# Kernel optimization log

Hardware: AMD Instinct MI355X
Metric: run time of the kernel (lower is better)

## Reference

```python
import jax, jax.numpy as jnp
import numpy as np

B, T, C, H = 4, 2048, 1024, 16
HD = C // H  # head dim = 64


def setup_inputs() -> dict:
    key = jax.random.key(0)
    ks = jax.random.split(key, 5)
    s = 1.0 / np.sqrt(C)
    return {
        "x": jax.random.normal(ks[0], (B, T, C), jnp.float32),
        "Wk": jax.random.normal(ks[1], (C, C), jnp.float32) * s,
        "bk": jnp.zeros((C,), jnp.float32),
        "Wq": jax.random.normal(ks[2], (C, C), jnp.float32) * s,
        "bq": jnp.zeros((C,), jnp.float32),
        "Wv": jax.random.normal(ks[3], (C, C), jnp.float32) * s,
        "bv": jnp.zeros((C,), jnp.float32),
        "Wp": jax.random.normal(ks[4], (C, C), jnp.float32) * s,
        "bp": jnp.zeros((C,), jnp.float32),
    }


def reference(x, Wk, bk, Wq, bq, Wv, bv, Wp, bp):
    # Linear(in, out): y = x @ W.T + b  (W stored as [out, in], torch convention)
    k = (x @ Wk.T + bk).reshape(B, T, H, HD).transpose(0, 2, 1, 3)  # [B,H,T,HD]
    q = (x @ Wq.T + bq).reshape(B, T, H, HD).transpose(0, 2, 1, 3)
    v = (x @ Wv.T + bv).reshape(B, T, H, HD).transpose(0, 2, 1, 3)
    scale = 1.0 / np.sqrt(HD)
    att = jnp.einsum("bhqd,bhkd->bhqk", q, k) * scale  # [B,H,T,T]
    causal = jnp.tril(jnp.ones((T, T), bool))
    att = jnp.where(causal[None, None, :, :], att, -jnp.inf)
    att = jax.nn.softmax(att, axis=-1)
    y = jnp.einsum("bhqk,bhkd->bhqd", att, v)  # [B,H,T,HD]
    y = y.transpose(0, 2, 1, 3).reshape(B, T, C)
    return y @ Wp.T + bp
```

## Files before the change

kernel.cpp:

```cpp
#include <hip/hip_runtime.h>
#include <hip/hip_bf16.h>
#include <cmath>

#define Tt 2048
#define Cc 1024
#define Hh 16
#define HDd 64

typedef __attribute__((ext_vector_type(8))) short short8;
typedef __attribute__((ext_vector_type(4))) float f32x4;

#define ASYNC16(gp, lp)                                       \
    __builtin_amdgcn_global_load_lds(                         \
        (const __attribute__((address_space(1))) void*)(gp),  \
        (__attribute__((address_space(3))) void*)(lp), 16, 0, 0)

__device__ __forceinline__ unsigned short f32_bf16(float f) {
    unsigned u = __float_as_uint(f);
    u += 0x7FFF + ((u >> 16) & 1);
    return (unsigned short)(u >> 16);
}
__device__ __forceinline__ unsigned short f32_bf16_rn(float f) {
    return (unsigned short)((__float_as_uint(f) + 0x8000u) >> 16);
}
__device__ __forceinline__ float fast_exp2(float x) {
#if __has_builtin(__builtin_amdgcn_exp2f)
    return __builtin_amdgcn_exp2f(x);
#else
    return exp2f(x);
#endif
}

__global__ __launch_bounds__(256) void cvt_all(
    const float* __restrict__ x, const float* __restrict__ a,
    const float* __restrict__ b, const float* __restrict__ c,
    const float* __restrict__ d, unsigned short* __restrict__ ox,
    unsigned short* __restrict__ oa, unsigned short* __restrict__ ob,
    unsigned short* __restrict__ oc, unsigned short* __restrict__ od) {
    const int id = blockIdx.x * 256 + threadIdx.x;
    const float* src; unsigned short* dst; int sub;
    if (id < 2097152) {
        src = x; dst = ox; sub = id;
    } else {
        const int wi = id - 2097152;
        const int which = wi >> 18;
        sub = wi & 262143;
        if (which == 0)      { src = a; dst = oa; }
        else if (which == 1) { src = b; dst = ob; }
        else if (which == 2) { src = c; dst = oc; }
        else                 { src = d; dst = od; }
    }
    float4 v = ((const float4*)src)[sub];
    ushort4 o;
    o.x = f32_bf16(v.x); o.y = f32_bf16(v.y);
    o.z = f32_bf16(v.z); o.w = f32_bf16(v.w);
    ((ushort4*)dst)[sub] = o;
}

__global__ __launch_bounds__(512, 2) void gemm_qkv8(
    const unsigned short* __restrict__ A,
    const unsigned short* __restrict__ Wcat,
    const float* __restrict__ bq, const float* __restrict__ bk,
    const float* __restrict__ bv,
    unsigned short* __restrict__ qout, unsigned short* __restrict__ kout,
    unsigned short* __restrict__ vout) {
    extern __shared__ unsigned short lds[];

    const int tid  = threadIdx.x;
    const int wid  = tid >> 6;
    const int lane = tid & 63;
    const int quad = lane >> 4;
    const int lr   = lane & 15;
    const int wr   = wid >> 2;
    const int wc   = wid & 3;

    const int bm0 = blockIdx.y * 256;
    const int bn0 = blockIdx.x * 256;

    const int srow  = wid * 8 + (lane >> 3);
    const int scol  = ((lane & 7) ^ (lane >> 3)) * 8;
    const int sldso = wid * 512;

    const int a_r   = wr * 64 + lr;
    const int b_r   = wc * 32 + lr;
    const int slot0 = (quad ^ (lr & 7)) * 8;
    const int slot1 = ((quad ^ 4) ^ (lr & 7)) * 8;

    f32x4 acc[8][4];
    const f32x4 zero = {0.f, 0.f, 0.f, 0.f};
#pragma unroll
    for (int i = 0; i < 8; ++i)
#pragma unroll
        for (int j = 0; j < 4; ++j) acc[i][j] = zero;

    short8 areg[4][2];
    short8 breg[2][2][2];

#define STG(S, BUF, REG, GB, GROW)                                          \
    do {                                                                    \
        if ((S) < 16) {                                                     \
            unsigned short* lb = lds + ((BUF) * 4 + (REG)) * 8192 + sldso;  \
            const unsigned short* gp =                                      \
                (GB) + (size_t)((GROW) + srow) * Cc + (S) * 64 + scol;      \
            ASYNC16(gp, lb);                                                \
            ASYNC16(gp + (size_t)64 * Cc, lb + 4096);                       \
        }                                                                   \
    } while (0)

#define LDA(mh)                                                             \
    do {                                                                    \
        const unsigned short* ab = bufb + (mh) * 8192;                      \
        _Pragma("unroll") for (int mf = 0; mf < 4; ++mf) {                  \
            areg[mf][0] = *(const short8*)(ab + (a_r + mf * 16) * 64 + slot0); \
            areg[mf][1] = *(const short8*)(ab + (a_r + mf * 16) * 64 + slot1); \
        }                                                                   \
    } while (0)

#define LDB(nh)                                                             \
    do {                                                                    \
        const unsigned short* bb = bufb + (2 + (nh)) * 8192;                \
        _Pragma("unroll") for (int nf = 0; nf < 2; ++nf) {                  \
            breg[nh][nf][0] = *(const short8*)(bb + (b_r + nf * 16) * 64 + slot0); \
            breg[nh][nf][1] = *(const short8*)(bb + (b_r + nf * 16) * 64 + slot1); \
        }                                                                   \
    } while (0)

#define MFMA_PHASE(mh, nh)                                                  \
    _Pragma("unroll") for (int mf = 0; mf < 4; ++mf)                        \
    _Pragma("unroll") for (int nf = 0; nf < 2; ++nf) {                      \
        acc[(mh)*4+mf][(nh)*2+nf] = __builtin_amdgcn_mfma_f32_16x16x32_bf16( \
            areg[mf][0], breg[nh][nf][0], acc[(mh)*4+mf][(nh)*2+nf], 0,0,0); \
        acc[(mh)*4+mf][(nh)*2+nf] = __builtin_amdgcn_mfma_f32_16x16x32_bf16( \
            areg[mf][1], breg[nh][nf][1], acc[(mh)*4+mf][(nh)*2+nf], 0,0,0); \
    }

#define TILE(T, BC, WN)                                                     \
    {                                                                       \
        const unsigned short* bufb = lds + (BC) * 32768;                    \
        LDA(0);                                                             \
        LDB(0);                                                             \
        STG((T) + 1, (BC) ^ 1, 1, A, bm0 + 128);                            \
        __builtin_amdgcn_s_barrier();                                       \
        asm volatile("s_waitcnt lgkmcnt(0)" ::: "memory");                  \
        __builtin_amdgcn_s_setprio(1);                                      \
        MFMA_PHASE(0, 0);                                                   \
        __builtin_amdgcn_s_setprio(0);                                      \
        __builtin_amdgcn_s_barrier();                                       \
        LDB(1);                                                             \
        STG((T) + 1, (BC) ^ 1, 3, Wcat, bn0 + 128);                         \
        __builtin_amdgcn_s_barrier();                                       \
        asm volatile("s_waitcnt lgkmcnt(0)" ::: "memory");                  \
        __builtin_amdgcn_s_setprio(1);                                      \
        MFMA_PHASE(0, 1);                                                   \
        __builtin_amdgcn_s_setprio(0);                                      \
        __builtin_amdgcn_s_barrier();                                       \
        LDA(1);                                                             \
        STG((T) + 2, (BC), 0, A, bm0);                                      \
        __builtin_amdgcn_s_barrier();                                       \
        asm volatile("s_waitcnt lgkmcnt(0)" ::: "memory");                  \
        __builtin_amdgcn_s_setprio(1);                                      \
        MFMA_PHASE(1, 0);                                                   \
        __builtin_amdgcn_s_setprio(0);                                      \
        __builtin_amdgcn_s_barrier();                                       \
        STG((T) + 2, (BC), 2, Wcat, bn0);                                   \
        __builtin_amdgcn_s_barrier();                                       \
        __builtin_amdgcn_s_setprio(1);                                      \
        MFMA_PHASE(1, 1);                                                   \
        __builtin_amdgcn_s_setprio(0);                                      \
        asm volatile("s_waitcnt vmcnt(" #WN ")" ::: "memory");              \
        __builtin_amdgcn_s_barrier();                                       \
    }

    STG(0, 0, 0, A, bm0);
    STG(0, 0, 1, A, bm0 + 128);
    STG(0, 0, 2, Wcat, bn0);
    STG(0, 0, 3, Wcat, bn0 + 128);
    STG(1, 1, 0, A, bm0);
    STG(1, 1, 2, Wcat, bn0);
    asm volatile("s_waitcnt vmcnt(4)" ::: "memory");
    __builtin_amdgcn_s_barrier();

    for (int t2 = 0; t2 < 7; ++t2) {
        const int T0 = t2 * 2;
        TILE(T0, 0, 4);
        TILE(T0 + 1, 1, 4);
    }
    TILE(14, 0, 0);
    TILE(15, 1, 0);

#undef TILE
#undef MFMA_PHASE
#undef LDB
#undef LDA
#undef STG

    const int which = bn0 >> 10;
    const float* bias = (which == 0) ? bq : (which == 1) ? bk : bv;
    unsigned short* outp = (which == 0) ? qout : (which == 1) ? kout : vout;
    const float scale = (which == 0) ? 0.1803368801111204f : 1.0f;
    const bool vmode = (which == 2);
    const int nb = bn0 & 1023;

#pragma unroll
    for (int nh = 0; nh < 2; ++nh)
#pragma unroll
        for (int nf = 0; nf < 2; ++nf) {
            const int nl = nb + nh * 128 + wc * 32 + nf * 16 + lr;
            const float bvv = bias[nl];
            const int h = nl >> 6, hd = nl & 63;
#pragma unroll
            for (int mh = 0; mh < 2; ++mh)
#pragma unroll
                for (int mf = 0; mf < 4; ++mf) {
                    const f32x4 a = acc[mh * 4 + mf][nh * 2 + nf];
                    const int m0 = bm0 + mh * 128 + wr * 64 + mf * 16 + quad * 4;
                    const int b = m0 >> 11, t0 = m0 & 2047;
                    if (vmode) {
                        ushort4 pk;
                        pk.x = f32_bf16_rn(a[0] + bvv);
                        pk.y = f32_bf16_rn(a[1] + bvv);
                        pk.z = f32_bf16_rn(a[2] + bvv);
                        pk.w = f32_bf16_rn(a[3] + bvv);
                        *(ushort4*)(outp + (((size_t)(b * Hh + h)) * HDd + hd) * Tt + t0) = pk;
                    } else {
#pragma unroll
                        for (int r = 0; r < 4; ++r) {
                            outp[(((size_t)(b * Hh + h)) * Tt + t0 + r) * HDd + hd] =
                                f32_bf16_rn((a[r] + bvv) * scale);
                        }
                    }
                }
        }
}

__global__ __launch_bounds__(256) void gemm_proj(const unsigned short* __restrict__ A,
                                                 const unsigned short* __restrict__ W,
                                                 const float* __restrict__ bias,
                                                 float* __restrict__ out) {
    __shared__ unsigned short sA[2][128 * 32];
    __shared__ unsigned short sB[2][64 * 32];

    const int tid  = threadIdx.x;
    const int bm0  = blockIdx.y * 128;
    const int bn0  = blockIdx.x * 64;
    const int wid  = tid >> 6;
    const int lane = tid & 63;
    const int quad = lane >> 4;
    const int lr   = lane & 15;
    const int wm   = (wid & 1) * 64;
    const int wn   = (wid >> 1) * 32;

    const int sr   = lane >> 2;
    const int scol = (lane & 3) * 8;
    const int row0 = wid * 16 + sr;
    const int row1 = 64 + wid * 16 + sr;
    const int lo0  = wid * 512;
    const int lo1  = (4 + wid) * 512;

    f32x4 acc[4][2];
    f32x4 zero = {0.f, 0.f, 0.f, 0.f};
#pragma unroll
    for (int i = 0; i < 4; i++)
#pragma unroll
        for (int j = 0; j < 2; j++) acc[i][j] = zero;

    ASYNC16(A + (size_t)(bm0 + row0) * Cc + scol, sA[0] + lo0);
    ASYNC16(A + (size_t)(bm0 + row1) * Cc + scol, sA[0] + lo1);
    ASYNC16(W + (size_t)(bn0 + row0) * Cc + scol, sB[0] + lo0);
    __syncthreads();

    for (int kt = 0; kt < Cc / 32; ++kt) {
        const int cur = kt & 1, nxt = cur ^ 1;
        if (kt + 1 < Cc / 32) {
            const int kb = (kt + 1) * 32;
            ASYNC16(A + (size_t)(bm0 + row0) * Cc + kb + scol, sA[nxt] + lo0);
            ASYNC16(A + (size_t)(bm0 + row1) * Cc + kb + scol, sA[nxt] + lo1);
            ASYNC16(W + (size_t)(bn0 + row0) * Cc + kb + scol, sB[nxt] + lo0);
        }

        short8 af[4], bf[2];
#pragma unroll
        for (int i = 0; i < 4; i++)
            af[i] = *(const short8*)(sA[cur] + (wm + i * 16 + lr) * 32 + quad * 8);
#pragma unroll
        for (int j = 0; j < 2; j++)
            bf[j] = *(const short8*)(sB[cur] + (wn + j * 16 + lr) * 32 + quad * 8);
#pragma unroll
        for (int i = 0; i < 4; i++)
#pragma unroll
            for (int j = 0; j < 2; j++)
                acc[i][j] = __builtin_amdgcn_mfma_f32_16x16x32_bf16(af[i], bf[j], acc[i][j], 0, 0, 0);

        __syncthreads();
    }

#pragma unroll
    for (int j = 0; j < 2; j++) {
        const int n = bn0 + wn + j * 16 + lr;
        const float bvv = bias[n];
#pragma unroll
        for (int i = 0; i < 4; i++)
#pragma unroll
            for (int r = 0; r < 4; r++) {
                const int m = bm0 + wm + i * 16 + quad * 4 + r;
                out[(size_t)m * Cc + n] = acc[i][j][r] + bvv;
            }
    }
}

__global__ __launch_bounds__(256) void attn(const unsigned short* __restrict__ q,
                                            const unsigned short* __restrict__ k,
                                            const unsigned short* __restrict__ vt,
                                            unsigned short* __restrict__ y) {
    __shared__ unsigned short sK[2][64 * 72];
    __shared__ unsigned short sV[2][64 * 72];
    __shared__ unsigned short sP[4][2][16 * 72];

    const int tid  = threadIdx.x;
    const int wid  = tid >> 6;
    const int lane = tid & 63;
    const int quad = lane >> 4;
    const int lr   = lane & 15;

    const int bh = blockIdx.x * 8 + (blockIdx.y & 7);
    const int qx = blockIdx.y >> 3;
    const size_t headq = (size_t)bh * Tt * HDd;
    const unsigned short* kg = k + headq;
    const unsigned short* vg = vt + headq;
    const int b = bh >> 4, h = bh & 15;

    const int rs0 = tid >> 3;
    const int es  = (tid & 7) * 8;

    f32x4 zero = {0.f, 0.f, 0.f, 0.f};

    for (int pass = 0; pass < 2; ++pass) {
        const int qt = pass ? (15 - qx) : qx;
        const int qb = qt * 128;
        const int ntiles = 2 * qt + 2;

        short8 qf[2][2];
#pragma unroll
        for (int s = 0; s < 2; s++) {
            const unsigned short* qp =
                q + headq + (size_t)(qb + s * 64 + wid * 16 + lr) * HDd;
            qf[s][0] = *(const short8*)(qp + quad * 8);
            qf[s][1] = *(const short8*)(qp + 32 + quad * 8);
        }

        f32x4 o[2][4];
        float l_run[2][4];
#pragma unroll
        for (int s = 0; s < 2; s++)
#pragma unroll
            for (int i = 0; i < 4; i++) { o[s][i] = zero; l_run[s][i] = 0.f; }

        uint4 ka0 = *(const uint4*)(kg + (size_t)(rs0)      * HDd + es);
        uint4 ka1 = *(const uint4*)(kg + (size_t)(rs0 + 32) * HDd + es);
        uint4 va0 = *(const uint4*)(vg + (size_t)(rs0)      * Tt + es);
        uint4 va1 = *(const uint4*)(vg + (size_t)(rs0 + 32) * Tt + es);
        *(uint4*)(sK[0] + rs0 * 72 + es)        = ka0;
        *(uint4*)(sK[0] + (rs0 + 32) * 72 + es) = ka1;
        *(uint4*)(sV[0] + rs0 * 72 + es)        = va0;
        *(uint4*)(sV[0] + (rs0 + 32) * 72 + es) = va1;
        __syncthreads();
        {
            const int kb2 = 64;
            ka0 = *(const uint4*)(kg + (size_t)(kb2 + rs0)      * HDd + es);
            ka1 = *(const uint4*)(kg + (size_t)(kb2 + rs0 + 32) * HDd + es);
            va0 = *(const uint4*)(vg + (size_t)(rs0)      * Tt + kb2 + es);
            va1 = *(const uint4*)(vg + (size_t)(rs0 + 32) * Tt + kb2 + es);
        }

        for (int kt = 0; kt < ntiles; ++kt) {
            const int cur = kt & 1, nxt = cur ^ 1;
            if (kt + 1 < ntiles) {
                *(uint4*)(sK[nxt] + rs0 * 72 + es)        = ka0;
                *(uint4*)(sK[nxt] + (rs0 + 32) * 72 + es) = ka1;
                *(uint4*)(sV[nxt] + rs0 * 72 + es)        = va0;
                *(uint4*)(sV[nxt] + (rs0 + 32) * 72 + es) = va1;
            }
            if (kt + 2 < ntiles) {
                const int kb2 = (kt + 2) * 64;
                ka0 = *(const uint4*)(kg + (size_t)(kb2 + rs0)      * HDd + es);
                ka1 = *(const uint4*)(kg + (size_t)(kb2 + rs0 + 32) * HDd + es);
                va0 = *(const uint4*)(vg + (size_t)(rs0)      * Tt + kb2 + es);
                va1 = *(const uint4*)(vg + (size_t)(rs0 + 32) * Tt + kb2 + es);
            }

            const unsigned short* bK = sK[cur];
            const unsigned short* bV = sV[cur];
            const int s_lo = (kt == ntiles - 1) ? 1 : 0;

            short8 kf[4][2];
#pragma unroll
            for (int nt = 0; nt < 4; nt++) {
                kf[nt][0] = *(const short8*)(bK + (nt * 16 + lr) * 72 + quad * 8);
                kf[nt][1] = *(const short8*)(bK + (nt * 16 + lr) * 72 + 32 + quad * 8);
            }

            f32x4 sc[2][4];
            __builtin_amdgcn_s_setprio(1);
#pragma unroll
            for (int s = 0; s < 2; s++) {
                if (s < s_lo) continue;
#pragma unroll
                for (int nt = 0; nt < 4; nt++) {
                    f32x4 a = zero;
                    a = __builtin_amdgcn_mfma_f32_16x16x32_bf16(qf[s][0], kf[nt][0], a, 0, 0, 0);
                    a = __builtin_amdgcn_mfma_f32_16x16x32_bf16(qf[s][1], kf[nt][1], a, 0, 0, 0);
                    sc[s][nt] = a;
                }
            }
            __builtin_amdgcn_s_setprio(0);

#pragma unroll
            for (int s = 0; s < 2; s++) {
                if (s < s_lo) continue;
                if (kt == ntiles - 2 + s) {
#pragma unroll
                    for (int nt = 0; nt < 4; nt++)
#pragma unroll
                        for (int r = 0; r < 4; r++)
                            sc[s][nt][r] = (nt * 16 + lr <= wid * 16 + quad * 4 + r)
                                               ? sc[s][nt][r] : -INFINITY;
                }
                unsigned short* sPw = sP[wid][s];
#pragma unroll
                for (int nt = 0; nt < 4; nt++)
#pragma unroll
                    for (int r = 0; r < 4; r++) {
                        const float p = fast_exp2(sc[s][nt][r]);
                        l_run[s][r] += p;
                        sPw[(quad * 4 + r) * 72 + nt * 16 + lr] = f32_bf16_rn(p);
                    }
            }

            short8 vf[4][2];
#pragma unroll
            for (int nt = 0; nt < 4; nt++) {
                vf[nt][0] = *(const short8*)(bV + (nt * 16 + lr) * 72 + quad * 8);
                vf[nt][1] = *(const short8*)(bV + (nt * 16 + lr) * 72 + 32 + quad * 8);
            }

            __builtin_amdgcn_s_setprio(1);
#pragma unroll
            for (int s = 0; s < 2; s++) {
                if (s < s_lo) continue;
                const unsigned short* sPw = sP[wid][s];
                short8 pa0 = *(const short8*)(sPw + lr * 72 + quad * 8);
                short8 pa1 = *(const short8*)(sPw + lr * 72 + 32 + quad * 8);
#pragma unroll
                for (int nt = 0; nt < 4; nt++) {
                    o[s][nt] = __builtin_amdgcn_mfma_f32_16x16x32_bf16(pa0, vf[nt][0], o[s][nt], 0, 0, 0);
                    o[s][nt] = __builtin_amdgcn_mfma_f32_16x16x32_bf16(pa1, vf[nt][1], o[s][nt], 0, 0, 0);
                }
            }
            __builtin_amdgcn_s_setprio(0);

            __syncthreads();
        }

#pragma unroll
        for (int s = 0; s < 2; s++) {
#pragma unroll
            for (int r = 0; r < 4; r++) {
                float ls = l_run[s][r];
                ls += __shfl_xor(ls, 1);
                ls += __shfl_xor(ls, 2);
                ls += __shfl_xor(ls, 4);
                ls += __shfl_xor(ls, 8);
                const float inv = 1.0f / ls;
                const int t = qb + s * 64 + wid * 16 + quad * 4 + r;
#pragma unroll
                for (int nt = 0; nt < 4; nt++) {
                    const int dim = nt * 16 + lr;
                    y[((size_t)(b * Tt + t)) * Cc + h * HDd + dim] =
                        f32_bf16_rn(o[s][nt][r] * inv);
                }
            }
        }
    }
}

extern "C" void kernel_launch(void* const* d_in, const int* in_sizes, int n_in,
                              void* d_out, int out_size, void* d_ws, size_t ws_size,
                              hipStream_t stream) {
    const float* x  = (const float*)d_in[0];
    const float* Wk = (const float*)d_in[1];
    const float* bk = (const float*)d_in[2];
    const float* Wq = (const float*)d_in[3];
    const float* bq = (const float*)d_in[4];
    const float* Wv = (const float*)d_in[5];
    const float* bv = (const float*)d_in[6];
    const float* Wp = (const float*)d_in[7];
    const float* bp = (const float*)d_in[8];
    float* out = (float*)d_out;

    char* ws = (char*)d_ws;
    size_t off = 0;
    auto alloc = [&](size_t bytes) { char* p = ws + off; off += bytes; return p; };
    const size_t MK = (size_t)8192 * 1024;
    const size_t NK = (size_t)1024 * 1024;
    unsigned short* xb   = (unsigned short*)alloc(MK * 2);
    unsigned short* Wcat = (unsigned short*)alloc(3 * NK * 2);
    unsigned short* Wqb  = Wcat;
    unsigned short* Wkb  = Wcat + NK;
    unsigned short* Wvb  = Wcat + 2 * NK;
    unsigned short* Wpb  = (unsigned short*)alloc(NK * 2);
    unsigned short* qh   = (unsigned short*)alloc(MK * 2);
    unsigned short* kh   = (unsigned short*)alloc(MK * 2);
    unsigned short* vth  = (unsigned short*)alloc(MK * 2);
    unsigned short* ya   = (unsigned short*)alloc(MK * 2);

    static bool lds_attr_set = false;
    if (!lds_attr_set) {
        (void)hipFuncSetAttribute((const void*)gemm_qkv8,
                                  hipFuncAttributeMaxDynamicSharedMemorySize,
                                  131072);
        lds_attr_set = true;
    }

    cvt_all<<<12288, 256, 0, stream>>>(x, Wq, Wk, Wv, Wp, xb, Wqb, Wkb, Wvb, Wpb);

    gemm_qkv8<<<dim3(12, 32), 512, 131072, stream>>>(xb, Wcat, bq, bk, bv, qh, kh, vth);

    attn<<<dim3(8, 64), 256, 0, stream>>>(qh, kh, vth, ya);

    gemm_proj<<<dim3(16, 64), 256, 0, stream>>>(ya, Wpb, bp, out);
}
```

Measured before the change: 265.4 us.

## Shrink attention query tile to 64 rows with async swizzled K/V staging

The attention kernel now gives each block 64 query rows instead of 128 and keeps the pass pairing for causal load balance. K/V tiles are staged directly into LDS with global_load_lds using an XOR-swizzled unpadded layout in place of register-staged padded copies, and the P buffer uses the same swizzle. The grid changes to 64x16 with launch_bounds(256,4), aiming to cut register and LDS pressure for higher occupancy and to avoid bank conflicts. In exchange, each K/V tile is reused by half as many queries, so total K/V traffic roughly doubles.

```diff
diff --git a/kernel.cpp b/kernel.cpp
--- a/kernel.cpp
+++ b/kernel.cpp
@@ -308,13 +308,13 @@
     }
 }
 
-__global__ __launch_bounds__(256) void attn(const unsigned short* __restrict__ q,
-                                            const unsigned short* __restrict__ k,
-                                            const unsigned short* __restrict__ vt,
-                                            unsigned short* __restrict__ y) {
-    __shared__ unsigned short sK[2][64 * 72];
-    __shared__ unsigned short sV[2][64 * 72];
-    __shared__ unsigned short sP[4][2][16 * 72];
+__global__ __launch_bounds__(256, 4) void attn(const unsigned short* __restrict__ q,
+                                               const unsigned short* __restrict__ k,
+                                               const unsigned short* __restrict__ vt,
+                                               unsigned short* __restrict__ y) {
+    __shared__ unsigned short sK[2][64 * 64];
+    __shared__ unsigned short sV[2][64 * 64];
+    __shared__ unsigned short sP[4][16 * 64];
 
     const int tid  = threadIdx.x;
     const int wid  = tid >> 6;
@@ -322,139 +322,112 @@
     const int quad = lane >> 4;
     const int lr   = lane & 15;
 
-    const int bh = blockIdx.x * 8 + (blockIdx.y & 7);
-    const int qx = blockIdx.y >> 3;
+    const int bh = blockIdx.x;
+    const int qx = blockIdx.y;
     const size_t headq = (size_t)bh * Tt * HDd;
     const unsigned short* kg = k + headq;
     const unsigned short* vg = vt + headq;
     const int b = bh >> 4, h = bh & 15;
 
-    const int rs0 = tid >> 3;
-    const int es  = (tid & 7) * 8;
-
-    f32x4 zero = {0.f, 0.f, 0.f, 0.f};
+    const int g_r = lane >> 3;
+    const int g_c = ((lane & 7) ^ g_r) * 8;
+    const unsigned short* kst = kg + (size_t)(wid * 16 + g_r) * HDd + g_c;
+    const unsigned short* vst = vg + (size_t)(wid * 16 + g_r) * Tt + g_c;
+    unsigned short* dK0 = sK[0] + wid * 1024;
+    unsigned short* dK1 = sK[1] + wid * 1024;
+    unsigned short* dV0 = sV[0] + wid * 1024;
+    unsigned short* dV1 = sV[1] + wid * 1024;
+
+#define STAGE_KV(BUF, KB)                                                   \
+    do {                                                                    \
+        unsigned short* dK = (BUF) ? dK1 : dK0;                             \
+        unsigned short* dV = (BUF) ? dV1 : dV0;                             \
+        ASYNC16(kst + (size_t)(KB) * HDd,       dK);                        \
+        ASYNC16(kst + (size_t)((KB) + 8) * HDd, dK + 512);                  \
+        ASYNC16(vst + (KB),                     dV);                        \
+        ASYNC16(vst + (size_t)8 * Tt + (KB),    dV + 512);                  \
+    } while (0)
+
+    const int fr_off = lr * 64 + ((quad ^ (lr & 7)) * 8);
+    const int hq8 = (((lr >> 3) ^ ((quad & 1) << 2)) * 8);
+    const int pwb = quad * 256 + (lr & 7);
+    unsigned short* sPw = sP[wid];
+
+    const f32x4 zero = {0.f, 0.f, 0.f, 0.f};
 
     for (int pass = 0; pass < 2; ++pass) {
-        const int qt = pass ? (15 - qx) : qx;
-        const int qb = qt * 128;
-        const int ntiles = 2 * qt + 2;
-
-        short8 qf[2][2];
-#pragma unroll
-        for (int s = 0; s < 2; s++) {
-            const unsigned short* qp =
-                q + headq + (size_t)(qb + s * 64 + wid * 16 + lr) * HDd;
-            qf[s][0] = *(const short8*)(qp + quad * 8);
-            qf[s][1] = *(const short8*)(qp + 32 + quad * 8);
-        }
-
-        f32x4 o[2][4];
-        float l_run[2][4];
-#pragma unroll
-        for (int s = 0; s < 2; s++)
-#pragma unroll
-            for (int i = 0; i < 4; i++) { o[s][i] = zero; l_run[s][i] = 0.f; }
-
-        uint4 ka0 = *(const uint4*)(kg + (size_t)(rs0)      * HDd + es);
-        uint4 ka1 = *(const uint4*)(kg + (size_t)(rs0 + 32) * HDd + es);
-        uint4 va0 = *(const uint4*)(vg + (size_t)(rs0)      * Tt + es);
-        uint4 va1 = *(const uint4*)(vg + (size_t)(rs0 + 32) * Tt + es);
-        *(uint4*)(sK[0] + rs0 * 72 + es)        = ka0;
-        *(uint4*)(sK[0] + (rs0 + 32) * 72 + es) = ka1;
-        *(uint4*)(sV[0] + rs0 * 72 + es)        = va0;
-        *(uint4*)(sV[0] + (rs0 + 32) * 72 + es) = va1;
+        const int qt = pass ? (31 - qx) : qx;
+        const int qb = qt * 64;
+        const int ntiles = qt + 1;
+
+        const unsigned short* qp = q + headq + (size_t)(qb + wid * 16 + lr) * HDd;
+        const short8 qf0 = *(const short8*)(qp + quad * 8);
+        const short8 qf1 = *(const short8*)(qp + 32 + quad * 8);
+
+        f32x4 o[4];
+        float l_run[4];
+#pragma unroll
+        for (int i = 0; i < 4; i++) { o[i] = zero; l_run[i] = 0.f; }
+
+        STAGE_KV(0, 0);
         __syncthreads();
-        {
-            const int kb2 = 64;
-            ka0 = *(const uint4*)(kg + (size_t)(kb2 + rs0)      * HDd + es);
-            ka1 = *(const uint4*)(kg + (size_t)(kb2 + rs0 + 32) * HDd + es);
-            va0 = *(const uint4*)(vg + (size_t)(rs0)      * Tt + kb2 + es);
-            va1 = *(const uint4*)(vg + (size_t)(rs0 + 32) * Tt + kb2 + es);
-        }
 
         for (int kt = 0; kt < ntiles; ++kt) {
-            const int cur = kt & 1, nxt = cur ^ 1;
-            if (kt + 1 < ntiles) {
-                *(uint4*)(sK[nxt] + rs0 * 72 + es)        = ka0;
-                *(uint4*)(sK[nxt] + (rs0 + 32) * 72 + es) = ka1;
-                *(uint4*)(sV[nxt] + rs0 * 72 + es)        = va0;
-                *(uint4*)(sV[nxt] + (rs0 + 32) * 72 + es) = va1;
-            }
-            if (kt + 2 < ntiles) {
-                const int kb2 = (kt + 2) * 64;
-                ka0 = *(const uint4*)(kg + (size_t)(kb2 + rs0)      * HDd + es);
-                ka1 = *(const uint4*)(kg + (size_t)(kb2 + rs0 + 32) * HDd + es);
-                va0 = *(const uint4*)(vg + (size_t)(rs0)      * Tt + kb2 + es);
-                va1 = *(const uint4*)(vg + (size_t)(rs0 + 32) * Tt + kb2 + es);
-            }
+            const int cur = kt & 1;
+            if (kt + 1 < ntiles) STAGE_KV(cur ^ 1, (kt + 1) * 64);
 
             const unsigned short* bK = sK[cur];
             const unsigned short* bV = sV[cur];
-            const int s_lo = (kt == ntiles - 1) ? 1 : 0;
 
             short8 kf[4][2];
 #pragma unroll
             for (int nt = 0; nt < 4; nt++) {
-                kf[nt][0] = *(const short8*)(bK + (nt * 16 + lr) * 72 + quad * 8);
-                kf[nt][1] = *(const short8*)(bK + (nt * 16 + lr) * 72 + 32 + quad * 8);
-            }
-
-            f32x4 sc[2][4];
+                kf[nt][0] = *(const short8*)(bK + nt * 1024 + fr_off);
+                kf[nt][1] = *(const short8*)(bK + nt * 1024 + (fr_off ^ 32));
+            }
+
+            f32x4 sc[4];
             __builtin_amdgcn_s_setprio(1);
 #pragma unroll
-            for (int s = 0; s < 2; s++) {
-                if (s < s_lo) continue;
-#pragma unroll
-                for (int nt = 0; nt < 4; nt++) {
-                    f32x4 a = zero;
-                    a = __builtin_amdgcn_mfma_f32_16x16x32_bf16(qf[s][0], kf[nt][0], a, 0, 0, 0);
-                    a = __builtin_amdgcn_mfma_f32_16x16x32_bf16(qf[s][1], kf[nt][1], a, 0, 0, 0);
-                    sc[s][nt] = a;
+            for (int nt = 0; nt < 4; nt++) {
+                f32x4 a = __builtin_amdgcn_mfma_f32_16x16x32_bf16(qf0, kf[nt][0], zero, 0, 0, 0);
+                sc[nt]  = __builtin_amdgcn_mfma_f32_16x16x32_bf16(qf1, kf[nt][1], a, 0, 0, 0);
+            }
+            __builtin_amdgcn_s_setprio(0);
+
+            short8 vf[4][2];
+#pragma unroll
+            for (int nt = 0; nt < 4; nt++) {
+                vf[nt][0] = *(const short8*)(bV + nt * 1024 + fr_off);
+                vf[nt][1] = *(const short8*)(bV + nt * 1024 + (fr_off ^ 32));
+            }
+
+            if (kt == qt) {
+#pragma unroll
+                for (int nt = 0; nt < 4; nt++)
+#pragma unroll
+                    for (int r = 0; r < 4; r++)
+                        sc[nt][r] = (nt * 16 + lr <= wid * 16 + quad * 4 + r)
+                                        ? sc[nt][r] : -INFINITY;
+            }
+
+#pragma unroll
+            for (int nt = 0; nt < 4; nt++)
+#pragma unroll
+                for (int r = 0; r < 4; r++) {
+                    const float p = fast_exp2(sc[nt][r]);
+                    l_run[r] += p;
+                    sPw[pwb + r * 64 + ((nt * 16 ^ r * 8) ^ hq8)] = f32_bf16_rn(p);
                 }
-            }
-            __builtin_amdgcn_s_setprio(0);
-
-#pragma unroll
-            for (int s = 0; s < 2; s++) {
-                if (s < s_lo) continue;
-                if (kt == ntiles - 2 + s) {
-#pragma unroll
-                    for (int nt = 0; nt < 4; nt++)
-#pragma unroll
-                        for (int r = 0; r < 4; r++)
-                            sc[s][nt][r] = (nt * 16 + lr <= wid * 16 + quad * 4 + r)
-                                               ? sc[s][nt][r] : -INFINITY;
-                }
-                unsigned short* sPw = sP[wid][s];
-#pragma unroll
-                for (int nt = 0; nt < 4; nt++)
-#pragma unroll
-                    for (int r = 0; r < 4; r++) {
-                        const float p = fast_exp2(sc[s][nt][r]);
-                        l_run[s][r] += p;
-                        sPw[(quad * 4 + r) * 72 + nt * 16 + lr] = f32_bf16_rn(p);
-                    }
-            }
-
-            short8 vf[4][2];
+
+            const short8 pa0 = *(const short8*)(sPw + fr_off);
+            const short8 pa1 = *(const short8*)(sPw + (fr_off ^ 32));
+
+            __builtin_amdgcn_s_setprio(1);
 #pragma unroll
             for (int nt = 0; nt < 4; nt++) {
-                vf[nt][0] = *(const short8*)(bV + (nt * 16 + lr) * 72 + quad * 8);
-                vf[nt][1] = *(const short8*)(bV + (nt * 16 + lr) * 72 + 32 + quad * 8);
-            }
-
-            __builtin_amdgcn_s_setprio(1);
-#pragma unroll
-            for (int s = 0; s < 2; s++) {
-                if (s < s_lo) continue;
-                const unsigned short* sPw = sP[wid][s];
-                short8 pa0 = *(const short8*)(sPw + lr * 72 + quad * 8);
-                short8 pa1 = *(const short8*)(sPw + lr * 72 + 32 + quad * 8);
-#pragma unroll
-                for (int nt = 0; nt < 4; nt++) {
-                    o[s][nt] = __builtin_amdgcn_mfma_f32_16x16x32_bf16(pa0, vf[nt][0], o[s][nt], 0, 0, 0);
-                    o[s][nt] = __builtin_amdgcn_mfma_f32_16x16x32_bf16(pa1, vf[nt][1], o[s][nt], 0, 0, 0);
-                }
+                o[nt] = __builtin_amdgcn_mfma_f32_16x16x32_bf16(pa0, vf[nt][0], o[nt], 0, 0, 0);
+                o[nt] = __builtin_amdgcn_mfma_f32_16x16x32_bf16(pa1, vf[nt][1], o[nt], 0, 0, 0);
             }
             __builtin_amdgcn_s_setprio(0);
 
@@ -462,25 +435,23 @@
         }
 
 #pragma unroll
-        for (int s = 0; s < 2; s++) {
-#pragma unroll
-            for (int r = 0; r < 4; r++) {
-                float ls = l_run[s][r];
-                ls += __shfl_xor(ls, 1);
-                ls += __shfl_xor(ls, 2);
-                ls += __shfl_xor(ls, 4);
-                ls += __shfl_xor(ls, 8);
-                const float inv = 1.0f / ls;
-                const int t = qb + s * 64 + wid * 16 + quad * 4 + r;
-#pragma unroll
-                for (int nt = 0; nt < 4; nt++) {
-                    const int dim = nt * 16 + lr;
-                    y[((size_t)(b * Tt + t)) * Cc + h * HDd + dim] =
-                        f32_bf16_rn(o[s][nt][r] * inv);
-                }
+        for (int r = 0; r < 4; r++) {
+            float ls = l_run[r];
+            ls += __shfl_xor(ls, 1);
+            ls += __shfl_xor(ls, 2);
+            ls += __shfl_xor(ls, 4);
+            ls += __shfl_xor(ls, 8);
+            const float inv = 1.0f / ls;
+            const int t = qb + wid * 16 + quad * 4 + r;
+#pragma unroll
+            for (int nt = 0; nt < 4; nt++) {
+                const int dim = nt * 16 + lr;
+                y[((size_t)(b * Tt + t)) * Cc + h * HDd + dim] =
+                    f32_bf16_rn(o[nt][r] * inv);
             }
         }
     }
+#undef STAGE_KV
 }
 
 extern "C" void kernel_launch(void* const* d_in, const int* in_sizes, int n_in,
@@ -525,7 +496,7 @@
 
     gemm_qkv8<<<dim3(12, 32), 512, 131072, stream>>>(xb, Wcat, bq, bk, bv, qh, kh, vth);
 
-    attn<<<dim3(8, 64), 256, 0, stream>>>(qh, kh, vth, ya);
+    attn<<<dim3(64, 16), 256, 0, stream>>>(qh, kh, vth, ya);
 
     gemm_proj<<<dim3(16, 64), 256, 0, stream>>>(ya, Wpb, bp, out);
 }
```

Result: faster. 259.3 us (-2.3%).
